# Kernel tuning notes

Measured on AMD Instinct MI355X. Metric: run time of the kernel, lower is better.

The kernel has to match this reference:

```python
import jax, jax.numpy as jnp
import numpy as np

FP8_E4M3_MAX = 448.0  # max representable magnitude in float8_e4m3fn


def setup_inputs() -> dict:
    key = jax.random.key(0)
    k1, k2, k3 = jax.random.split(key, 3)
    n_tokens, d_in, d_out = 8192, 4096, 16384
    x = jax.random.normal(k1, (n_tokens, d_in), dtype=jnp.float32)
    # weight stored in fp8 domain (values stand in for dequantized-by-scale fp8 codes)
    weight = jax.random.normal(k2, (d_out, d_in), dtype=jnp.float32)
    bias = jax.random.normal(k3, (d_out,), dtype=jnp.float32) * 0.1
    input_scale = jnp.float32(0.05)   # per-tensor activation scale
    weight_scale = jnp.float32(0.01)  # per-tensor weight scale
    return {"x": x, "weight": weight, "bias": bias,
            "input_scale": input_scale, "weight_scale": weight_scale}


def reference(x, weight, bias, input_scale, weight_scale):
    # fp8 qdq path: quantize activation to fp8 e4m3 domain (fake-quant: scale + clamp),
    # then scaled GEMM: out = (x_q @ W_q^T) * (input_scale * weight_scale) + bias,
    # matching cublas_scaled_mm(input, weight.t(), scale_a, scale_b) + bias.
    x_q = jnp.clip(x / input_scale, -FP8_E4M3_MAX, FP8_E4M3_MAX)  # [T, d_in]
    acc = jnp.einsum('ti,oi->to', x_q, weight)                     # [T, d_out]
    out = acc * (input_scale * weight_scale) + bias
    return out
```

## Files before the change

### kernel.cpp

```cpp
#include <hip/hip_runtime.h>
#include <stdint.h>
#include <stddef.h>


typedef _Float16 half8 __attribute__((ext_vector_type(8)));
typedef _Float16 half4v __attribute__((ext_vector_type(4)));
typedef float f32x4 __attribute__((ext_vector_type(4)));

#define BM 256
#define BN 256
#define BK 32
#define NBUF 4
#define FP8MAX 448.0f

__device__ __forceinline__ void gload_lds16(const _Float16* g, _Float16* lds) {
  __builtin_amdgcn_global_load_lds(
      (const __attribute__((address_space(1))) uint32_t*)g,
      (__attribute__((address_space(3))) uint32_t*)lds, 16, 0, 0);
}

#define BAR() asm volatile("s_barrier" ::: "memory")
#define WAIT_VM(N) asm volatile("s_waitcnt vmcnt(" #N ")" ::: "memory")
#define LGKM0() asm volatile("s_waitcnt lgkmcnt(0)" ::: "memory")

#define MFMA16(AF, BF, ACC) do {                                              \
  __builtin_amdgcn_s_setprio(1);                                              \
  _Pragma("unroll")                                                           \
  for (int m_ = 0; m_ < 4; ++m_) {                                            \
    _Pragma("unroll")                                                         \
    for (int n_ = 0; n_ < 4; ++n_)                                            \
      ACC[m_][n_] = __builtin_amdgcn_mfma_f32_16x16x32_f16(                   \
          AF[m_], BF[n_], ACC[m_][n_], 0, 0, 0);                              \
  }                                                                           \
  __builtin_amdgcn_s_setprio(0);                                              \
} while (0)

__global__ void cvt_x_kernel(const float* __restrict__ x, _Float16* __restrict__ xq,
                             const float* __restrict__ s_ptr, long n4) {
  float inv = 1.0f / s_ptr[0];
  long i = (long)blockIdx.x * blockDim.x + threadIdx.x;
  long stride = (long)gridDim.x * blockDim.x;
  const float4* x4 = (const float4*)x;
  for (long j = i; j < n4; j += stride) {
    float4 v = x4[j];
    half4v h;
    h[0] = (_Float16)fminf(fmaxf(v.x * inv, -FP8MAX), FP8MAX);
    h[1] = (_Float16)fminf(fmaxf(v.y * inv, -FP8MAX), FP8MAX);
    h[2] = (_Float16)fminf(fmaxf(v.z * inv, -FP8MAX), FP8MAX);
    h[3] = (_Float16)fminf(fmaxf(v.w * inv, -FP8MAX), FP8MAX);
    *(half4v*)(xq + j * 4) = h;
  }
}

__global__ void cvt_w_kernel(const float* __restrict__ w, _Float16* __restrict__ wq,
                             long n4) {
  long i = (long)blockIdx.x * blockDim.x + threadIdx.x;
  long stride = (long)gridDim.x * blockDim.x;
  const float4* w4 = (const float4*)w;
  for (long j = i; j < n4; j += stride) {
    float4 v = w4[j];
    half4v h;
    h[0] = (_Float16)v.x; h[1] = (_Float16)v.y;
    h[2] = (_Float16)v.z; h[3] = (_Float16)v.w;
    *(half4v*)(wq + j * 4) = h;
  }
}

__global__ __launch_bounds__(512, 2)
void gemm256_fr(const _Float16* __restrict__ A, const _Float16* __restrict__ B,
                const float* __restrict__ bias, const float* __restrict__ is_ptr,
                const float* __restrict__ ws_ptr, float* __restrict__ out,
                int M, int N, int K) {
  __shared__ __align__(16) _Float16 lds[NBUF][32][512];

  const int nbn = N / BN;
  const int nwg = gridDim.x;
  int wg = blockIdx.x;
  if ((nwg & 7) == 0) {
    int q = nwg >> 3;
    wg = (wg & 7) * q + (wg >> 3);
  }
  const int brow = (wg / nbn) * BM;
  const int bcol = (wg % nbn) * BN;

  const int tid  = threadIdx.x;
  const int lane = tid & 63;
  const int w    = tid >> 6;
  const int wr   = w >> 2;
  const int wc   = w & 3;

  const size_t laneoff = (size_t)(lane & 15) * K + (size_t)(lane >> 4) * 8;
  const int blk0 = w * 4;
  const _Float16* gsrc[4];
#pragma unroll
  for (int j = 0; j < 4; ++j) {
    int b = blk0 + j;
    if (b < 16)
      gsrc[j] = A + (size_t)(brow + (b >> 3) * 128 + (b & 7) * 16) * K + laneoff;
    else
      gsrc[j] = B + (size_t)(bcol + ((b - 16) >> 2) * 64 + ((b - 16) & 3) * 16) * K + laneoff;
  }

  auto stage2 = [&](int tb, int kt, int j0) {
#pragma unroll
    for (int j = 0; j < 2; ++j)
      gload_lds16(gsrc[j0 + j] + kt, &lds[tb][blk0 + j0 + j][0]);
  };

  f32x4 accL[4][4] = {};
  f32x4 accH[4][4] = {};

  const int NT = K / BK;

  stage2(0, 0, 0);      stage2(0, 0, 2);
  stage2(1, BK, 0);     stage2(1, BK, 2);
  stage2(2, 2 * BK, 0); stage2(2, 2 * BK, 2);
  WAIT_VM(8);
  BAR();

  for (int t = 0; t < NT; ++t) {
    const int cur = t & 3;
    const bool pf = (t + 3) < NT;
    const int pb = (t + 3) & 3;
    const int pk = (t + 3) * BK;
    half8 a[4], b[4];

#pragma unroll
    for (int m = 0; m < 4; ++m) a[m] = *(const half8*)&lds[cur][wr * 8 + m][lane * 8];
#pragma unroll
    for (int n = 0; n < 4; ++n) b[n] = *(const half8*)&lds[cur][16 + wc * 4 + n][lane * 8];
    if (pf) stage2(pb, pk, 0);
    BAR();
    LGKM0();
    MFMA16(a, b, accL);
    BAR();

#pragma unroll
    for (int m = 0; m < 4; ++m) a[m] = *(const half8*)&lds[cur][wr * 8 + 4 + m][lane * 8];
    if (pf) stage2(pb, pk, 2);
    BAR();
    LGKM0();
    MFMA16(a, b, accH);
    if (t < NT - 3)       WAIT_VM(8);
    else if (t == NT - 3) WAIT_VM(4);
    else if (t == NT - 2) WAIT_VM(0);
    BAR();
  }

  const float sc = is_ptr[0] * ws_ptr[0];
  const int orow = brow + wr * 128;
  const int ocol = bcol + wc * 64;
#pragma unroll
  for (int n = 0; n < 4; ++n) {
    const int col = ocol + n * 16 + (lane & 15);
    const float bv = bias[col];
#pragma unroll
    for (int m = 0; m < 4; ++m) {
#pragma unroll
      for (int r = 0; r < 4; ++r) {
        const int row = orow + m * 16 + (lane >> 4) * 4 + r;
        out[(size_t)row * N + col] = accL[m][n][r] * sc + bv;
        out[(size_t)(row + 64) * N + col] = accH[m][n][r] * sc + bv;
      }
    }
  }
}

extern "C" void kernel_launch(void* const* d_in, const int* in_sizes, int n_in,
                              void* d_out, int out_size, void* d_ws, size_t ws_size,
                              hipStream_t stream) {
  const float* x    = (const float*)d_in[0];
  const float* wgt  = (const float*)d_in[1];
  const float* bias = (const float*)d_in[2];
  const float* is   = (const float*)d_in[3];
  const float* wsc  = (const float*)d_in[4];
  float* out = (float*)d_out;

  const long x_n = in_sizes[0];
  const long w_n = in_sizes[1];
  const int  N   = in_sizes[2];
  const int  K   = (int)(w_n / N);
  const int  M   = (int)(x_n / K);

  _Float16* xq = (_Float16*)d_ws;
  _Float16* wq = xq + x_n;

  cvt_x_kernel<<<2048, 256, 0, stream>>>(x, xq, is, x_n >> 2);
  cvt_w_kernel<<<2048, 256, 0, stream>>>(wgt, wq, w_n >> 2);

  const int nwg = (M / BM) * (N / BN);
  gemm256_fr<<<nwg, 512, 0, stream>>>(xq, wq, bias, is, wsc, out, M, N, K);
}
```

Baseline: 1.365 ms.

## Software-pipeline LDS fragment loads and cut GEMM loop to one barrier per tile

Restructures the GEMM main loop so the next K-tile's A/B fragments are read from LDS into registers while the current tile's MFMAs run. Ping-pong register sets are used, with the loop unrolled by two. All four global-to-LDS loads for a tile are issued together. The four barriers per K-step become a single barrier, with partial lgkmcnt waits and sched_barrier fences controlling the overlap. This targets barrier stalls and LDS read latency exposed before each MFMA block, at the cost of extra register pressure and the assumption that the tile count is even.

```diff
diff --git a/kernel.cpp b/kernel.cpp
--- a/kernel.cpp
+++ b/kernel.cpp
@@ -21,7 +21,8 @@
 
 #define BAR() asm volatile("s_barrier" ::: "memory")
 #define WAIT_VM(N) asm volatile("s_waitcnt vmcnt(" #N ")" ::: "memory")
-#define LGKM0() asm volatile("s_waitcnt lgkmcnt(0)" ::: "memory")
+#define WAIT_LGKM(N) asm volatile("s_waitcnt lgkmcnt(" #N ")" ::: "memory")
+#define SCHED_FENCE() __builtin_amdgcn_sched_barrier(0)
 
 #define MFMA16(AF, BF, ACC) do {                                              \
   __builtin_amdgcn_s_setprio(1);                                              \
@@ -67,7 +68,7 @@
 }
 
 __global__ __launch_bounds__(512, 2)
-void gemm256_fr(const _Float16* __restrict__ A, const _Float16* __restrict__ B,
+void gemm256_rp(const _Float16* __restrict__ A, const _Float16* __restrict__ B,
                 const float* __restrict__ bias, const float* __restrict__ is_ptr,
                 const float* __restrict__ ws_ptr, float* __restrict__ out,
                 int M, int N, int K) {
@@ -101,10 +102,10 @@
       gsrc[j] = B + (size_t)(bcol + ((b - 16) >> 2) * 64 + ((b - 16) & 3) * 16) * K + laneoff;
   }
 
-  auto stage2 = [&](int tb, int kt, int j0) {
-#pragma unroll
-    for (int j = 0; j < 2; ++j)
-      gload_lds16(gsrc[j0 + j] + kt, &lds[tb][blk0 + j0 + j][0]);
+  auto stage = [&](int tb, int kt) {
+#pragma unroll
+    for (int j = 0; j < 4; ++j)
+      gload_lds16(gsrc[j] + kt, &lds[tb][blk0 + j][0]);
   };
 
   f32x4 accL[4][4] = {};
@@ -112,39 +113,48 @@
 
   const int NT = K / BK;
 
-  stage2(0, 0, 0);      stage2(0, 0, 2);
-  stage2(1, BK, 0);     stage2(1, BK, 2);
-  stage2(2, 2 * BK, 0); stage2(2, 2 * BK, 2);
-  WAIT_VM(8);
+  auto tile_body = [&](int t, half8 (&AC)[4], half8 (&BC)[4],
+                       half8 (&AN)[4], half8 (&BN_)[4]) {
+    const int cb = t & 3, nb = (t + 1) & 3;
+    const bool pf = (t + 3) < NT;
+    half8 AH[4];
+    if (pf) stage((t + 3) & 3, (t + 3) * BK);
+#pragma unroll
+    for (int m = 0; m < 4; ++m)
+      AH[m] = *(const half8*)&lds[cb][wr * 8 + 4 + m][lane * 8];
+    MFMA16(AC, BC, accL);
+#pragma unroll
+    for (int m = 0; m < 4; ++m)
+      AN[m] = *(const half8*)&lds[nb][wr * 8 + m][lane * 8];
+#pragma unroll
+    for (int n = 0; n < 4; ++n)
+      BN_[n] = *(const half8*)&lds[nb][16 + wc * 4 + n][lane * 8];
+    WAIT_LGKM(8);
+    SCHED_FENCE();
+    MFMA16(AH, BC, accH);
+    WAIT_LGKM(0);
+    SCHED_FENCE();
+    if (pf) { WAIT_VM(4); } else { WAIT_VM(0); }
+    BAR();
+  };
+
+  stage(0, 0);
+  stage(1, BK);
+  stage(2, 2 * BK);
+  WAIT_VM(4);
   BAR();
 
-  for (int t = 0; t < NT; ++t) {
-    const int cur = t & 3;
-    const bool pf = (t + 3) < NT;
-    const int pb = (t + 3) & 3;
-    const int pk = (t + 3) * BK;
-    half8 a[4], b[4];
-
-#pragma unroll
-    for (int m = 0; m < 4; ++m) a[m] = *(const half8*)&lds[cur][wr * 8 + m][lane * 8];
-#pragma unroll
-    for (int n = 0; n < 4; ++n) b[n] = *(const half8*)&lds[cur][16 + wc * 4 + n][lane * 8];
-    if (pf) stage2(pb, pk, 0);
-    BAR();
-    LGKM0();
-    MFMA16(a, b, accL);
-    BAR();
-
-#pragma unroll
-    for (int m = 0; m < 4; ++m) a[m] = *(const half8*)&lds[cur][wr * 8 + 4 + m][lane * 8];
-    if (pf) stage2(pb, pk, 2);
-    BAR();
-    LGKM0();
-    MFMA16(a, b, accH);
-    if (t < NT - 3)       WAIT_VM(8);
-    else if (t == NT - 3) WAIT_VM(4);
-    else if (t == NT - 2) WAIT_VM(0);
-    BAR();
+  half8 aP[4], bP[4], aQ[4], bQ[4];
+#pragma unroll
+  for (int m = 0; m < 4; ++m) aP[m] = *(const half8*)&lds[0][wr * 8 + m][lane * 8];
+#pragma unroll
+  for (int n = 0; n < 4; ++n) bP[n] = *(const half8*)&lds[0][16 + wc * 4 + n][lane * 8];
+  WAIT_LGKM(0);
+  SCHED_FENCE();
+
+  for (int t = 0; t < NT; t += 2) {
+    tile_body(t,     aP, bP, aQ, bQ);
+    tile_body(t + 1, aQ, bQ, aP, bP);
   }
 
   const float sc = is_ptr[0] * ws_ptr[0];
@@ -189,5 +199,5 @@
   cvt_w_kernel<<<2048, 256, 0, stream>>>(wgt, wq, w_n >> 2);
 
   const int nwg = (M / BM) * (N / BN);
-  gemm256_fr<<<nwg, 512, 0, stream>>>(xq, wq, bias, is, wsc, out, M, N, K);
-}
+  gemm256_rp<<<nwg, 512, 0, stream>>>(xq, wq, bias, is, wsc, out, M, N, K);
+}
```

Result: no change. 1.360 ms (-0.4%).

## Shrink GEMM tile to 128x256 with 3-stage pipeline and higher occupancy

Applied to the files above, without the earlier changes.

Replaces the 256x256 tile with two accumulator halves by a 128x256 tile using a single accumulator set. LDS buffering drops from 4 to 3 stages and launch bounds target 4 workgroups per CU. The per-iteration barrier count falls from four to one, and the tile-to-workgroup mapping switches to column-major. The aim is more waves in flight and less barrier overhead, at the cost of lower arithmetic intensity per tile and more global/L2 traffic for B.

```diff
diff --git a/kernel.cpp b/kernel.cpp
--- a/kernel.cpp
+++ b/kernel.cpp
@@ -7,10 +7,11 @@
 typedef _Float16 half4v __attribute__((ext_vector_type(4)));
 typedef float f32x4 __attribute__((ext_vector_type(4)));
 
-#define BM 256
+#define BM 128
 #define BN 256
 #define BK 32
-#define NBUF 4
+#define NBUF 3
+#define NBLK 24
 #define FP8MAX 448.0f
 
 __device__ __forceinline__ void gload_lds16(const _Float16* g, _Float16* lds) {
@@ -22,6 +23,7 @@
 #define BAR() asm volatile("s_barrier" ::: "memory")
 #define WAIT_VM(N) asm volatile("s_waitcnt vmcnt(" #N ")" ::: "memory")
 #define LGKM0() asm volatile("s_waitcnt lgkmcnt(0)" ::: "memory")
+#define SCHED_FENCE() __builtin_amdgcn_sched_barrier(0)
 
 #define MFMA16(AF, BF, ACC) do {                                              \
   __builtin_amdgcn_s_setprio(1);                                              \
@@ -66,22 +68,22 @@
   }
 }
 
-__global__ __launch_bounds__(512, 2)
-void gemm256_fr(const _Float16* __restrict__ A, const _Float16* __restrict__ B,
-                const float* __restrict__ bias, const float* __restrict__ is_ptr,
-                const float* __restrict__ ws_ptr, float* __restrict__ out,
-                int M, int N, int K) {
-  __shared__ __align__(16) _Float16 lds[NBUF][32][512];
+__global__ __launch_bounds__(512, 4)
+void gemm128x256(const _Float16* __restrict__ A, const _Float16* __restrict__ B,
+                 const float* __restrict__ bias, const float* __restrict__ is_ptr,
+                 const float* __restrict__ ws_ptr, float* __restrict__ out,
+                 int M, int N, int K) {
+  __shared__ __align__(16) _Float16 lds[NBUF][NBLK * 512];
 
-  const int nbn = N / BN;
+  const int nbm = M / BM;
   const int nwg = gridDim.x;
   int wg = blockIdx.x;
   if ((nwg & 7) == 0) {
     int q = nwg >> 3;
     wg = (wg & 7) * q + (wg >> 3);
   }
-  const int brow = (wg / nbn) * BM;
-  const int bcol = (wg % nbn) * BN;
+  const int brow = (wg % nbm) * BM;
+  const int bcol = (wg / nbm) * BN;
 
   const int tid  = threadIdx.x;
   const int lane = tid & 63;
@@ -90,65 +92,56 @@
   const int wc   = w & 3;
 
   const size_t laneoff = (size_t)(lane & 15) * K + (size_t)(lane >> 4) * 8;
-  const int blk0 = w * 4;
-  const _Float16* gsrc[4];
+  const int blk0 = w * 3;
+  const _Float16* gsrc[3];
 #pragma unroll
-  for (int j = 0; j < 4; ++j) {
+  for (int j = 0; j < 3; ++j) {
     int b = blk0 + j;
-    if (b < 16)
-      gsrc[j] = A + (size_t)(brow + (b >> 3) * 128 + (b & 7) * 16) * K + laneoff;
+    if (b < 8)
+      gsrc[j] = A + (size_t)(brow + b * 16) * K + laneoff;
     else
-      gsrc[j] = B + (size_t)(bcol + ((b - 16) >> 2) * 64 + ((b - 16) & 3) * 16) * K + laneoff;
+      gsrc[j] = B + (size_t)(bcol + (b - 8) * 16) * K + laneoff;
   }
 
-  auto stage2 = [&](int tb, int kt, int j0) {
+  auto stage = [&](int tb, int kt) {
 #pragma unroll
-    for (int j = 0; j < 2; ++j)
-      gload_lds16(gsrc[j0 + j] + kt, &lds[tb][blk0 + j0 + j][0]);
+    for (int j = 0; j < 3; ++j)
+      gload_lds16(gsrc[j] + kt, &lds[tb][(blk0 + j) * 512]);
   };
 
-  f32x4 accL[4][4] = {};
-  f32x4 accH[4][4] = {};
+  f32x4 acc[4][4] = {};
 
   const int NT = K / BK;
 
-  stage2(0, 0, 0);      stage2(0, 0, 2);
-  stage2(1, BK, 0);     stage2(1, BK, 2);
-  stage2(2, 2 * BK, 0); stage2(2, 2 * BK, 2);
-  WAIT_VM(8);
+  stage(0, 0);
+  stage(1, BK);
+  WAIT_VM(3);
   BAR();
 
+  int cur = 0;
   for (int t = 0; t < NT; ++t) {
-    const int cur = t & 3;
-    const bool pf = (t + 3) < NT;
-    const int pb = (t + 3) & 3;
-    const int pk = (t + 3) * BK;
     half8 a[4], b[4];
-
 #pragma unroll
-    for (int m = 0; m < 4; ++m) a[m] = *(const half8*)&lds[cur][wr * 8 + m][lane * 8];
+    for (int m = 0; m < 4; ++m)
+      a[m] = *(const half8*)&lds[cur][(wr * 4 + m) * 512 + lane * 8];
 #pragma unroll
-    for (int n = 0; n < 4; ++n) b[n] = *(const half8*)&lds[cur][16 + wc * 4 + n][lane * 8];
-    if (pf) stage2(pb, pk, 0);
-    BAR();
+    for (int n = 0; n < 4; ++n)
+      b[n] = *(const half8*)&lds[cur][(8 + wc * 4 + n) * 512 + lane * 8];
+    if (t + 2 < NT) {
+      int sb = cur + 2; if (sb >= NBUF) sb -= NBUF;
+      stage(sb, (t + 2) * BK);
+    }
     LGKM0();
-    MFMA16(a, b, accL);
-    BAR();
-
-#pragma unroll
-    for (int m = 0; m < 4; ++m) a[m] = *(const half8*)&lds[cur][wr * 8 + 4 + m][lane * 8];
-    if (pf) stage2(pb, pk, 2);
-    BAR();
-    LGKM0();
-    MFMA16(a, b, accH);
-    if (t < NT - 3)       WAIT_VM(8);
-    else if (t == NT - 3) WAIT_VM(4);
+    SCHED_FENCE();
+    MFMA16(a, b, acc);
+    if (t < NT - 2)       WAIT_VM(3);
     else if (t == NT - 2) WAIT_VM(0);
     BAR();
+    ++cur; if (cur >= NBUF) cur -= NBUF;
   }
 
   const float sc = is_ptr[0] * ws_ptr[0];
-  const int orow = brow + wr * 128;
+  const int orow = brow + wr * 64;
   const int ocol = bcol + wc * 64;
 #pragma unroll
   for (int n = 0; n < 4; ++n) {
@@ -159,8 +152,7 @@
 #pragma unroll
       for (int r = 0; r < 4; ++r) {
         const int row = orow + m * 16 + (lane >> 4) * 4 + r;
-        out[(size_t)row * N + col] = accL[m][n][r] * sc + bv;
-        out[(size_t)(row + 64) * N + col] = accH[m][n][r] * sc + bv;
+        out[(size_t)row * N + col] = acc[m][n][r] * sc + bv;
       }
     }
   }
@@ -189,5 +181,5 @@
   cvt_w_kernel<<<2048, 256, 0, stream>>>(wgt, wq, w_n >> 2);
 
   const int nwg = (M / BM) * (N / BN);
-  gemm256_fr<<<nwg, 512, 0, stream>>>(xq, wq, bias, is, wsc, out, M, N, K);
+  gemm128x256<<<nwg, 512, 0, stream>>>(xq, wq, bias, is, wsc, out, M, N, K);
 }
```

Measured after the change: 1.742 ms. +27.5%, slower.

## Restructure GEMM mainloop with BK=64, XOR-swizzled LDS and split A/B staging

Applied to the files above, without the earlier changes.

Replaces the 4-buffer BK=32 fragment-ordered LDS layout with BK=64 double-buffered A and B tiles stored row-major with an XOR swizzle. Each k-tile is split into four quadrant MFMA phases, with B for the next tile and A two tiles ahead staged in between. The goal is fewer barriers per unit of K, bank-conflict-free fragment reads, and better overlap of global-to-LDS loads with MFMA work. The cost is more register pressure from holding eight A fragments, and a delicate vmcnt and barrier schedule, since A is staged into the buffer currently being read.

```diff
diff --git a/kernel.cpp b/kernel.cpp
--- a/kernel.cpp
+++ b/kernel.cpp
@@ -9,8 +9,7 @@
 
 #define BM 256
 #define BN 256
-#define BK 32
-#define NBUF 4
+#define BK 64
 #define FP8MAX 448.0f
 
 __device__ __forceinline__ void gload_lds16(const _Float16* g, _Float16* lds) {
@@ -22,15 +21,21 @@
 #define BAR() asm volatile("s_barrier" ::: "memory")
 #define WAIT_VM(N) asm volatile("s_waitcnt vmcnt(" #N ")" ::: "memory")
 #define LGKM0() asm volatile("s_waitcnt lgkmcnt(0)" ::: "memory")
-
-#define MFMA16(AF, BF, ACC) do {                                              \
+#define SCHED_FENCE() __builtin_amdgcn_sched_barrier(0)
+
+#define MFMA_Q(AF, BF, MG, NG) do {                                           \
   __builtin_amdgcn_s_setprio(1);                                              \
   _Pragma("unroll")                                                           \
-  for (int m_ = 0; m_ < 4; ++m_) {                                            \
+  for (int mf_ = 0; mf_ < 4; ++mf_) {                                         \
     _Pragma("unroll")                                                         \
-    for (int n_ = 0; n_ < 4; ++n_)                                            \
-      ACC[m_][n_] = __builtin_amdgcn_mfma_f32_16x16x32_f16(                   \
-          AF[m_], BF[n_], ACC[m_][n_], 0, 0, 0);                              \
+    for (int nf_ = 0; nf_ < 2; ++nf_) {                                       \
+      _Pragma("unroll")                                                       \
+      for (int ks_ = 0; ks_ < 2; ++ks_)                                       \
+        acc[(MG)*4 + mf_][(NG)*2 + nf_] =                                     \
+            __builtin_amdgcn_mfma_f32_16x16x32_f16(                           \
+                AF[mf_*2 + ks_], BF[nf_*2 + ks_],                             \
+                acc[(MG)*4 + mf_][(NG)*2 + nf_], 0, 0, 0);                    \
+    }                                                                         \
   }                                                                           \
   __builtin_amdgcn_s_setprio(0);                                              \
 } while (0)
@@ -67,11 +72,12 @@
 }
 
 __global__ __launch_bounds__(512, 2)
-void gemm256_fr(const _Float16* __restrict__ A, const _Float16* __restrict__ B,
+void gemm256_sw(const _Float16* __restrict__ A, const _Float16* __restrict__ B,
                 const float* __restrict__ bias, const float* __restrict__ is_ptr,
                 const float* __restrict__ ws_ptr, float* __restrict__ out,
                 int M, int N, int K) {
-  __shared__ __align__(16) _Float16 lds[NBUF][32][512];
+  __shared__ __align__(16) _Float16 sA[2][256 * 64];
+  __shared__ __align__(16) _Float16 sB[2][256 * 64];
 
   const int nbn = N / BN;
   const int nwg = gridDim.x;
@@ -89,60 +95,81 @@
   const int wr   = w >> 2;
   const int wc   = w & 3;
 
-  const size_t laneoff = (size_t)(lane & 15) * K + (size_t)(lane >> 4) * 8;
-  const int blk0 = w * 4;
-  const _Float16* gsrc[4];
-#pragma unroll
-  for (int j = 0; j < 4; ++j) {
-    int b = blk0 + j;
-    if (b < 16)
-      gsrc[j] = A + (size_t)(brow + (b >> 3) * 128 + (b & 7) * 16) * K + laneoff;
-    else
-      gsrc[j] = B + (size_t)(bcol + ((b - 16) >> 2) * 64 + ((b - 16) & 3) * 16) * K + laneoff;
-  }
-
-  auto stage2 = [&](int tb, int kt, int j0) {
-#pragma unroll
-    for (int j = 0; j < 2; ++j)
-      gload_lds16(gsrc[j0 + j] + kt, &lds[tb][blk0 + j0 + j][0]);
-  };
-
-  f32x4 accL[4][4] = {};
-  f32x4 accH[4][4] = {};
-
+  const size_t lsrc = (size_t)(lane >> 3) * K + (size_t)((lane & 7) ^ (lane >> 3)) * 8;
+  const _Float16* gA = A + (size_t)brow * K + lsrc;
+  const _Float16* gB = B + (size_t)bcol * K + lsrc;
+
+  auto stageA = [&](int buf, int pi, int kt) {
+    gload_lds16(gA + (size_t)(pi * 64 + w * 8) * K + kt,
+                &sA[buf][(pi * 512 + w * 64) * 8]);
+  };
+  auto stageB = [&](int buf, int pi, int kt) {
+    gload_lds16(gB + (size_t)(pi * 64 + w * 8) * K + kt,
+                &sB[buf][(pi * 512 + w * 64) * 8]);
+  };
+
+  const int rdbase = (lane & 15) * 64;
+  const int e0 = rdbase + (((lane >> 4) + 0) ^ (lane & 7)) * 8;
+  const int e1 = rdbase + (((lane >> 4) + 4) ^ (lane & 7)) * 8;
+
+  auto ldA = [&](int buf, int mg, half8* a) {
+#pragma unroll
+    for (int mf = 0; mf < 4; ++mf) {
+      const int base = (wr * 8 + mg * 4 + mf) * 1024;
+      a[mf * 2 + 0] = *(const half8*)&sA[buf][base + e0];
+      a[mf * 2 + 1] = *(const half8*)&sA[buf][base + e1];
+    }
+  };
+  auto ldB = [&](int buf, int ng, half8* b) {
+#pragma unroll
+    for (int nf = 0; nf < 2; ++nf) {
+      const int base = (wc * 4 + ng * 2 + nf) * 1024;
+      b[nf * 2 + 0] = *(const half8*)&sB[buf][base + e0];
+      b[nf * 2 + 1] = *(const half8*)&sB[buf][base + e1];
+    }
+  };
+
+  f32x4 acc[8][4] = {};
   const int NT = K / BK;
 
-  stage2(0, 0, 0);      stage2(0, 0, 2);
-  stage2(1, BK, 0);     stage2(1, BK, 2);
-  stage2(2, 2 * BK, 0); stage2(2, 2 * BK, 2);
-  WAIT_VM(8);
+  stageA(0, 0, 0); stageA(0, 1, 0); stageA(0, 2, 0); stageA(0, 3, 0);
+  stageB(0, 0, 0); stageB(0, 1, 0); stageB(0, 2, 0); stageB(0, 3, 0);
+  stageA(1, 0, BK); stageA(1, 1, BK); stageA(1, 2, BK); stageA(1, 3, BK);
+  WAIT_VM(4);
   BAR();
 
   for (int t = 0; t < NT; ++t) {
-    const int cur = t & 3;
-    const bool pf = (t + 3) < NT;
-    const int pb = (t + 3) & 3;
-    const int pk = (t + 3) * BK;
-    half8 a[4], b[4];
-
-#pragma unroll
-    for (int m = 0; m < 4; ++m) a[m] = *(const half8*)&lds[cur][wr * 8 + m][lane * 8];
-#pragma unroll
-    for (int n = 0; n < 4; ++n) b[n] = *(const half8*)&lds[cur][16 + wc * 4 + n][lane * 8];
-    if (pf) stage2(pb, pk, 0);
-    BAR();
-    LGKM0();
-    MFMA16(a, b, accL);
-    BAR();
-
-#pragma unroll
-    for (int m = 0; m < 4; ++m) a[m] = *(const half8*)&lds[cur][wr * 8 + 4 + m][lane * 8];
-    if (pf) stage2(pb, pk, 2);
-    BAR();
-    LGKM0();
-    MFMA16(a, b, accH);
-    if (t < NT - 3)       WAIT_VM(8);
-    else if (t == NT - 3) WAIT_VM(4);
+    const int cur = t & 1, nxt = cur ^ 1;
+    const int ktB = (t + 1) * BK;
+    const int ktA = (t + 2) * BK;
+    const bool sb = (t + 1) < NT;
+    const bool sa = (t + 2) < NT;
+    half8 aL[8], aH[8], bL[4], bH[4];
+
+    ldA(cur, 0, aL); ldB(cur, 0, bL);
+    if (sb) { stageB(nxt, 0, ktB); stageB(nxt, 1, ktB); }
+    BAR();
+    LGKM0(); SCHED_FENCE();
+    MFMA_Q(aL, bL, 0, 0);
+    BAR();
+
+    ldA(cur, 1, aH);
+    if (sb) { stageB(nxt, 2, ktB); stageB(nxt, 3, ktB); }
+    BAR();
+    LGKM0(); SCHED_FENCE();
+    MFMA_Q(aH, bL, 1, 0);
+    BAR();
+
+    ldB(cur, 1, bH);
+    if (sa) { stageA(cur, 0, ktA); stageA(cur, 1, ktA); }
+    BAR();
+    LGKM0(); SCHED_FENCE();
+    MFMA_Q(aH, bH, 1, 1);
+    BAR();
+
+    if (sa) { stageA(cur, 2, ktA); stageA(cur, 3, ktA); }
+    MFMA_Q(aL, bH, 0, 1);
+    if (t < NT - 2)       WAIT_VM(4);
     else if (t == NT - 2) WAIT_VM(0);
     BAR();
   }
@@ -155,12 +182,11 @@
     const int col = ocol + n * 16 + (lane & 15);
     const float bv = bias[col];
 #pragma unroll
-    for (int m = 0; m < 4; ++m) {
+    for (int m = 0; m < 8; ++m) {
 #pragma unroll
       for (int r = 0; r < 4; ++r) {
         const int row = orow + m * 16 + (lane >> 4) * 4 + r;
-        out[(size_t)row * N + col] = accL[m][n][r] * sc + bv;
-        out[(size_t)(row + 64) * N + col] = accH[m][n][r] * sc + bv;
+        out[(size_t)row * N + col] = acc[m][n][r] * sc + bv;
       }
     }
   }
@@ -189,5 +215,5 @@
   cvt_w_kernel<<<2048, 256, 0, stream>>>(wgt, wq, w_n >> 2);
 
   const int nwg = (M / BM) * (N / BN);
-  gemm256_fr<<<nwg, 512, 0, stream>>>(xq, wq, bias, is, wsc, out, M, N, K);
-}
+  gemm256_sw<<<nwg, 512, 0, stream>>>(xq, wq, bias, is, wsc, out, M, N, K);
+}
```

New measurement: 1.270 ms. 7.0% less time.
